# Kernel tuning notes

Hardware: AMD Instinct MI355X
Metric: run time of the kernel (lower is better)

The kernel has to match this reference:

```python
import jax, jax.numpy as jnp
import numpy as np

RESERVOIR = 8192
INPUT_DIM = 64
DYN_LEN = 1000
PRED_LEN = 1000
SEQ_LEN = DYN_LEN + PRED_LEN


def setup_inputs() -> dict:
    key = jax.random.key(0)
    k1, k2, k3, k4 = jax.random.split(key, 4)
    return {
        "input_sequence": jax.random.normal(k1, (SEQ_LEN, INPUT_DIM), dtype=jnp.float32),
        "W_in": jax.random.normal(k2, (RESERVOIR, INPUT_DIM), dtype=jnp.float32) * 0.1,
        "W_h": jax.random.normal(k3, (RESERVOIR, RESERVOIR), dtype=jnp.float32) * (0.6 / np.sqrt(RESERVOIR)),
        "W_out": jax.random.normal(k4, (INPUT_DIM, RESERVOIR), dtype=jnp.float32) * 0.01,
        "dynamics_length": DYN_LEN,
        "iterative_prediction_length": PRED_LEN,
    }


def reference(input_sequence, W_in, W_h, W_out, dynamics_length, iterative_prediction_length):
    R = W_h.shape[0]
    even_mask = (jnp.arange(R) % 2) == 0  # augmentHidden: square even-indexed units

    def aug(h):
        return jnp.where(even_mask, h * h, h)

    # Warm-up (teacher-forced) phase: h_{t+1} = tanh(W_in x_t + W_h h_t), out = W_out aug(h)
    def warm_step(h, x):
        h = jnp.tanh(W_in @ x + W_h @ h)
        return h, W_out @ aug(h)

    h0 = jnp.zeros((R,), dtype=input_sequence.dtype)
    h, prediction_warm_up = jax.lax.scan(warm_step, h0, input_sequence[:dynamics_length])

    def pred_step(h, _):
        out = W_out @ aug(h)
        h = jnp.tanh(W_in @ out + W_h @ h)
        return h, out

    _, prediction = jax.lax.scan(pred_step, h, None, length=iterative_prediction_length)

    target = input_sequence[dynamics_length:]
    prediction_augment = jnp.concatenate([prediction_warm_up, prediction], axis=0)
    target_augment = input_sequence
    return prediction, target, prediction_augment, target_augment
```

## Files before the change

kernel.cpp:

```cpp
#include <hip/hip_runtime.h>
#include <hip/hip_fp16.h>
#include <stdint.h>

#define RES      8192
#define IN_DIM   64
#define DYN      1000
#define TOT      2000

#define BLOCKS   512
#define TPB      1024
#define WPB      16

#define WS_H0     0
#define WS_H1     8192
#define WS_OUT    16384
#define WS_DONE   16448
#define WS_FLAG   18496
#define WS_GEN    19520
#define WS_SLOT   20544
#define WS_TOTAL  36928
#define WS_WH16   40960

__global__ void copy_targets(const float* __restrict__ input, float* __restrict__ out) {
    int i = blockIdx.x * blockDim.x + threadIdx.x;
    if (i < 64000)  out[64000 + i]  = input[64000 + i];
    if (i < 128000) out[256000 + i] = input[i];
}

__global__ void convert_wh(const float* __restrict__ W_h, __half2* __restrict__ w16) {
    const float4* src = (const float4*)W_h;
    const int stride = gridDim.x * blockDim.x;
    for (int j = blockIdx.x * blockDim.x + threadIdx.x;
         j < RES * RES / 4; j += stride) {
        float4 v = src[j];
        w16[2 * j]     = __floats2half2_rn(v.x, v.y);
        w16[2 * j + 1] = __floats2half2_rn(v.z, v.w);
    }
}

__device__ __forceinline__ unsigned ld_u32(const unsigned* p) {
    return __hip_atomic_load(p, __ATOMIC_RELAXED, __HIP_MEMORY_SCOPE_AGENT);
}
__device__ __forceinline__ void st_u32(unsigned* p, unsigned v) {
    __hip_atomic_store(p, v, __ATOMIC_RELAXED, __HIP_MEMORY_SCOPE_AGENT);
}
__device__ __forceinline__ float ld_f32(const float* p) {
    return __hip_atomic_load(p, __ATOMIC_RELAXED, __HIP_MEMORY_SCOPE_AGENT);
}
__device__ __forceinline__ void st_f32(float* p, float v) {
    __hip_atomic_store(p, v, __ATOMIC_RELAXED, __HIP_MEMORY_SCOPE_AGENT);
}
__device__ __forceinline__ uint64_t ld_u64(const uint64_t* p) {
    return __hip_atomic_load(p, __ATOMIC_RELAXED, __HIP_MEMORY_SCOPE_AGENT);
}

template <bool FP16>
__global__ __launch_bounds__(TPB, 8) void esn_kernel(
    const float* __restrict__ input,
    const float* __restrict__ W_in,
    const float* __restrict__ W_h,
    const float* __restrict__ W_out,
    float* __restrict__ out,
    float* __restrict__ ws)
{
    __shared__ __align__(16) float h_lds[RES];
    __shared__ float xbuf[IN_DIM];

    float*    hbuf0  = ws + WS_H0;
    float*    hbuf1  = ws + WS_H1;
    float*    outbuf = ws + WS_OUT;
    unsigned* done   = (unsigned*)(ws + WS_DONE);
    unsigned* flag   = (unsigned*)(ws + WS_FLAG);
    unsigned* gen    = (unsigned*)(ws + WS_GEN);
    unsigned* slot   = (unsigned*)(ws + WS_SLOT);
    const __half2* wh16 = (const __half2*)(ws + WS_WH16);

    float* pred    = out;
    float* aug_out = out + 128000;

    const int tid  = threadIdx.x;
    const int lane = tid & 63;
    const int wid  = tid >> 6;
    const int bid  = blockIdx.x;
    const int r    = bid * WPB + wid;

    for (int t = 0; t < TOT; ++t) {
        const float* hcur = (t & 1) ? hbuf1 : hbuf0;
        float*       hnxt = (t & 1) ? hbuf0 : hbuf1;

        {
            const uint64_t* src = (const uint64_t*)hcur;
            uint64_t*       dst = (uint64_t*)h_lds;
            #pragma unroll
            for (int i = 0; i < RES / 2 / TPB; ++i)
                dst[tid + i * TPB] = ld_u64(src + tid + i * TPB);
        }
        __syncthreads();

        if (wid == 1 && bid < 64 && t >= 1) {
            const int j = bid;
            const float* wrow = W_out + (size_t)j * RES;
            float acc = 0.f;
            #pragma unroll 8
            for (int i = 0; i < RES / 256; ++i) {
                const int k = (lane << 2) + (i << 8);
                float4 w = *(const float4*)(wrow + k);
                float4 h = *(const float4*)(h_lds + k);
                acc += w.x * h.x * h.x + w.y * h.y + w.z * h.z * h.z + w.w * h.w;
            }
            #pragma unroll
            for (int off = 32; off; off >>= 1) acc += __shfl_xor(acc, off, 64);
            if (lane == 0) {
                if (t <= DYN)  aug_out[(size_t)(t - 1) * 64 + j] = acc;
                if (t >= DYN) {
                    pred[(size_t)(t - DYN) * 64 + j] = acc;
                    aug_out[(size_t)t * 64 + j]      = acc;
                    st_f32(outbuf + j, acc);
                    __builtin_amdgcn_s_waitcnt(0);
                    st_u32(done + j * 32, (unsigned)(t - DYN + 1));
                }
            }
        }

        if (wid == 0 && bid == 64 && t >= DYN && t < TOT - 1) {
            const unsigned p = (unsigned)(t - DYN + 1);
            for (;;) {
                unsigned v = ld_u32(done + lane * 32);
                if (__all((int)(v >= p))) break;
                __builtin_amdgcn_s_sleep(2);
            }
            __builtin_amdgcn_s_waitcnt(0);
            if (lane < 32) st_u32(flag + lane * 32, p);
        }

        if (t == TOT - 1) break;

        {
            float a0 = 0.f, a1 = 0.f, a2 = 0.f, a3 = 0.f;
            if (FP16) {
                const __half2* wrow = wh16 + (size_t)r * (RES / 2);
                #pragma unroll 8
                for (int i = 0; i < RES / 512; ++i) {
                    const int k = (lane << 2) + (i << 8);
                    const __half2 w0 = wrow[k + 0];
                    const __half2 w1 = wrow[k + 1];
                    const __half2 w2 = wrow[k + 2];
                    const __half2 w3 = wrow[k + 3];
                    float4 hA = *(const float4*)(h_lds + 2 * k);
                    float4 hB = *(const float4*)(h_lds + 2 * k + 4);
                    float2 f0 = __half22float2(w0);
                    float2 f1 = __half22float2(w1);
                    float2 f2 = __half22float2(w2);
                    float2 f3 = __half22float2(w3);
                    a0 += f0.x * hA.x; a1 += f0.y * hA.y;
                    a2 += f1.x * hA.z; a3 += f1.y * hA.w;
                    a0 += f2.x * hB.x; a1 += f2.y * hB.y;
                    a2 += f3.x * hB.z; a3 += f3.y * hB.w;
                }
            } else {
                const float* wrow = W_h + (size_t)r * RES;
                #pragma unroll 8
                for (int i = 0; i < RES / 256; ++i) {
                    const int k = (lane << 2) + (i << 8);
                    float4 w = *(const float4*)(wrow + k);
                    float4 h = *(const float4*)(h_lds + k);
                    a0 += w.x * h.x; a1 += w.y * h.y;
                    a2 += w.z * h.z; a3 += w.w * h.w;
                }
            }
            float acc = (a0 + a2) + (a1 + a3);

            float x_l;
            if (t < DYN) {
                x_l = input[(size_t)t * IN_DIM + lane];
            } else {
                const unsigned p = (unsigned)(t - DYN + 1);
                __syncthreads();
                if (tid == 0) {
                    while (ld_u32(flag + (bid & 31) * 32) < p)
                        __builtin_amdgcn_s_sleep(2);
                }
                __syncthreads();
                if (tid < IN_DIM) xbuf[tid] = ld_f32(outbuf + tid);
                __syncthreads();
                x_l = xbuf[lane];
            }
            acc += W_in[(size_t)r * IN_DIM + lane] * x_l;

            #pragma unroll
            for (int off = 32; off; off >>= 1) acc += __shfl_xor(acc, off, 64);
            if (lane == 0) st_f32(hnxt + r, tanhf(acc));
        }

        __builtin_amdgcn_s_waitcnt(0);
        __syncthreads();
        const unsigned e = (unsigned)(t + 1);
        if (tid == 0) st_u32(slot + bid * 32, e);
        if (bid == 0) {
            unsigned v = e;
            for (;;) {
                if (tid < BLOCKS) v = ld_u32(slot + tid * 32);
                if (__syncthreads_and(tid >= BLOCKS || v >= e)) break;
                __builtin_amdgcn_s_sleep(2);
            }
            if (tid < 32) st_u32(gen + tid * 32, e);
        } else {
            if (tid == 0) {
                while (ld_u32(gen + (bid & 31) * 32) < e)
                    __builtin_amdgcn_s_sleep(4);
            }
            __syncthreads();
        }
    }
}

extern "C" void kernel_launch(void* const* d_in, const int* in_sizes, int n_in,
                              void* d_out, int out_size, void* d_ws, size_t ws_size,
                              hipStream_t stream) {
    const float* input = (const float*)d_in[0];
    const float* W_in  = (const float*)d_in[1];
    const float* W_h   = (const float*)d_in[2];
    const float* W_out = (const float*)d_in[3];
    float* out = (float*)d_out;
    float* ws  = (float*)d_ws;

    hipMemsetAsync(d_ws, 0, WS_TOTAL * sizeof(float), stream);

    copy_targets<<<dim3((128000 + 255) / 256), dim3(256), 0, stream>>>(input, out);

    const size_t need = (size_t)WS_WH16 * sizeof(float)
                      + (size_t)RES * RES * sizeof(__half);
    if (ws_size >= need) {
        convert_wh<<<dim3(2048), dim3(1024), 0, stream>>>(
            W_h, (__half2*)(ws + WS_WH16));
        esn_kernel<true><<<dim3(BLOCKS), dim3(TPB), 0, stream>>>(
            input, W_in, W_h, W_out, out, ws);
    } else {
        esn_kernel<false><<<dim3(BLOCKS), dim3(TPB), 0, stream>>>(
            input, W_in, W_h, W_out, out, ws);
    }
}
```

Baseline: 74.22 ms.

## Halve grid to 256 blocks with two recurrent rows per wave

The grid drops from 512 to 256 blocks and each wave now computes two rows of W_h, sharing the LDS reads of h between both rows. The W_in weights are loaded once into registers before the time loop, and the two tanh results are written with one 64-bit store. Fewer blocks means less grid-barrier traffic and fewer per-step LDS refills of h, but each wave now carries twice the weight-streaming work and more registers, and launch bounds are lowered to 4.

Result: faster. 60.99 ms (-17.8%).

```diff
diff --git a/kernel.cpp b/kernel.cpp
--- a/kernel.cpp
+++ b/kernel.cpp
@@ -1,15 +1,16 @@
 #include <hip/hip_runtime.h>
 #include <hip/hip_fp16.h>
 #include <stdint.h>
+#include <string.h>
 
 #define RES      8192
 #define IN_DIM   64
 #define DYN      1000
 #define TOT      2000
 
-#define BLOCKS   512
+#define BLOCKS   256
 #define TPB      1024
-#define WPB      16
+#define ROWS_PB  32
 
 #define WS_H0     0
 #define WS_H1     8192
@@ -50,12 +51,15 @@
 __device__ __forceinline__ void st_f32(float* p, float v) {
     __hip_atomic_store(p, v, __ATOMIC_RELAXED, __HIP_MEMORY_SCOPE_AGENT);
 }
+__device__ __forceinline__ void st_u64(uint64_t* p, uint64_t v) {
+    __hip_atomic_store(p, v, __ATOMIC_RELAXED, __HIP_MEMORY_SCOPE_AGENT);
+}
 __device__ __forceinline__ uint64_t ld_u64(const uint64_t* p) {
     return __hip_atomic_load(p, __ATOMIC_RELAXED, __HIP_MEMORY_SCOPE_AGENT);
 }
 
 template <bool FP16>
-__global__ __launch_bounds__(TPB, 8) void esn_kernel(
+__global__ __launch_bounds__(TPB, 4) void esn_kernel(
     const float* __restrict__ input,
     const float* __restrict__ W_in,
     const float* __restrict__ W_h,
@@ -82,7 +86,13 @@
     const int lane = tid & 63;
     const int wid  = tid >> 6;
     const int bid  = blockIdx.x;
-    const int r    = bid * WPB + wid;
+    const int r0   = bid * ROWS_PB + wid * 2;
+
+    const float w_in0 = W_in[(size_t)r0 * IN_DIM + lane];
+    const float w_in1 = W_in[(size_t)(r0 + 1) * IN_DIM + lane];
+
+    const __half2* wr0 = wh16 + (size_t)r0 * (RES / 2);
+    const __half2* wr1 = wr0 + (RES / 2);
 
     for (int t = 0; t < TOT; ++t) {
         const float* hcur = (t & 1) ? hbuf1 : hbuf0;
@@ -136,39 +146,49 @@
         if (t == TOT - 1) break;
 
         {
-            float a0 = 0.f, a1 = 0.f, a2 = 0.f, a3 = 0.f;
+            float a00 = 0.f, a01 = 0.f, a02 = 0.f, a03 = 0.f;
+            float a10 = 0.f, a11 = 0.f, a12 = 0.f, a13 = 0.f;
             if (FP16) {
-                const __half2* wrow = wh16 + (size_t)r * (RES / 2);
                 #pragma unroll 8
                 for (int i = 0; i < RES / 512; ++i) {
                     const int k = (lane << 2) + (i << 8);
-                    const __half2 w0 = wrow[k + 0];
-                    const __half2 w1 = wrow[k + 1];
-                    const __half2 w2 = wrow[k + 2];
-                    const __half2 w3 = wrow[k + 3];
+                    const __half2 w00 = wr0[k + 0];
+                    const __half2 w01 = wr0[k + 1];
+                    const __half2 w02 = wr0[k + 2];
+                    const __half2 w03 = wr0[k + 3];
+                    const __half2 w10 = wr1[k + 0];
+                    const __half2 w11 = wr1[k + 1];
+                    const __half2 w12 = wr1[k + 2];
+                    const __half2 w13 = wr1[k + 3];
                     float4 hA = *(const float4*)(h_lds + 2 * k);
                     float4 hB = *(const float4*)(h_lds + 2 * k + 4);
-                    float2 f0 = __half22float2(w0);
-                    float2 f1 = __half22float2(w1);
-                    float2 f2 = __half22float2(w2);
-                    float2 f3 = __half22float2(w3);
-                    a0 += f0.x * hA.x; a1 += f0.y * hA.y;
-                    a2 += f1.x * hA.z; a3 += f1.y * hA.w;
-                    a0 += f2.x * hB.x; a1 += f2.y * hB.y;
-                    a2 += f3.x * hB.z; a3 += f3.y * hB.w;
+                    float2 f;
+                    f = __half22float2(w00); a00 += f.x * hA.x; a01 += f.y * hA.y;
+                    f = __half22float2(w01); a02 += f.x * hA.z; a03 += f.y * hA.w;
+                    f = __half22float2(w02); a00 += f.x * hB.x; a01 += f.y * hB.y;
+                    f = __half22float2(w03); a02 += f.x * hB.z; a03 += f.y * hB.w;
+                    f = __half22float2(w10); a10 += f.x * hA.x; a11 += f.y * hA.y;
+                    f = __half22float2(w11); a12 += f.x * hA.z; a13 += f.y * hA.w;
+                    f = __half22float2(w12); a10 += f.x * hB.x; a11 += f.y * hB.y;
+                    f = __half22float2(w13); a12 += f.x * hB.z; a13 += f.y * hB.w;
                 }
             } else {
-                const float* wrow = W_h + (size_t)r * RES;
+                const float* wrowA = W_h + (size_t)r0 * RES;
+                const float* wrowB = wrowA + RES;
                 #pragma unroll 8
                 for (int i = 0; i < RES / 256; ++i) {
                     const int k = (lane << 2) + (i << 8);
-                    float4 w = *(const float4*)(wrow + k);
+                    float4 w0 = *(const float4*)(wrowA + k);
+                    float4 w1 = *(const float4*)(wrowB + k);
                     float4 h = *(const float4*)(h_lds + k);
-                    a0 += w.x * h.x; a1 += w.y * h.y;
-                    a2 += w.z * h.z; a3 += w.w * h.w;
-                }
-            }
-            float acc = (a0 + a2) + (a1 + a3);
+                    a00 += w0.x * h.x; a01 += w0.y * h.y;
+                    a02 += w0.z * h.z; a03 += w0.w * h.w;
+                    a10 += w1.x * h.x; a11 += w1.y * h.y;
+                    a12 += w1.z * h.z; a13 += w1.w * h.w;
+                }
+            }
+            float acc0 = (a00 + a02) + (a01 + a03);
+            float acc1 = (a10 + a12) + (a11 + a13);
 
             float x_l;
             if (t < DYN) {
@@ -185,11 +205,22 @@
                 __syncthreads();
                 x_l = xbuf[lane];
             }
-            acc += W_in[(size_t)r * IN_DIM + lane] * x_l;
+            acc0 += w_in0 * x_l;
+            acc1 += w_in1 * x_l;
 
             #pragma unroll
-            for (int off = 32; off; off >>= 1) acc += __shfl_xor(acc, off, 64);
-            if (lane == 0) st_f32(hnxt + r, tanhf(acc));
+            for (int off = 32; off; off >>= 1) {
+                acc0 += __shfl_xor(acc0, off, 64);
+                acc1 += __shfl_xor(acc1, off, 64);
+            }
+            if (lane == 0) {
+                float2 hv;
+                hv.x = tanhf(acc0);
+                hv.y = tanhf(acc1);
+                uint64_t u;
+                memcpy(&u, &hv, 8);
+                st_u64((uint64_t*)(hnxt + r0), u);
+            }
         }
 
         __builtin_amdgcn_s_waitcnt(0);
```
